# Optimization experiments

Measured on AMD Instinct MI355X. Metric: run time of the kernel, lower is better.

The kernel has to match this reference:

```python
import jax, jax.numpy as jnp
import numpy as np

HIDDEN = 1024
FFN = 3584
NUM_EXPERTS = 8
TOP_K = 2
B, S = 2, 1024


def setup_inputs() -> dict:
    key = jax.random.key(0)
    k0, k1, k2, k3 = jax.random.split(key, 4)
    hidden_states = jax.random.normal(k0, (B, S, HIDDEN), dtype=jnp.float32)
    # torch Linear stores [out, in]; we keep gate as [E, H] (matches nn.Linear weight)
    gate_w = jax.random.normal(k1, (NUM_EXPERTS, HIDDEN), dtype=jnp.float32) * 0.02
    # GroupedLinear weights stored as [E, in, out] for direct x @ W per expert
    w_gate_up = jax.random.normal(k2, (NUM_EXPERTS, HIDDEN, 2 * FFN), dtype=jnp.float32) * 0.02
    w_down = jax.random.normal(k3, (NUM_EXPERTS, FFN, HIDDEN), dtype=jnp.float32) * 0.02
    return {"hidden_states": hidden_states, "gate_w": gate_w,
            "w_gate_up": w_gate_up, "w_down": w_down}


def reference(hidden_states, gate_w, w_gate_up, w_down):
    b, s, h = hidden_states.shape
    x = hidden_states.reshape(-1, h)                      # [T, H]
    T = x.shape[0]
    E = gate_w.shape[0]

    # Router: logits -> fp32 softmax -> top-k -> renormalize (Mixtral semantics)
    router_logits = x @ gate_w.T                          # [T, E]
    probs = jax.nn.softmax(router_logits.astype(jnp.float32), axis=-1)
    top_vals, top_idx = jax.lax.top_k(probs, TOP_K)       # [T, K]
    top_vals = top_vals / top_vals.sum(axis=-1, keepdims=True)
    top_vals = top_vals.astype(x.dtype)

    # Dense combine weights [T, E]: scatter top-k probs to expert slots.
    # Equivalent to permute -> grouped GEMM -> unpermute-with-probs.
    combine = jnp.zeros((T, E), dtype=x.dtype).at[
        jnp.arange(T)[:, None], top_idx].add(top_vals)

    out = jnp.zeros_like(x)
    for e in range(E):  # fixed small expert count
        gu = x @ w_gate_up[e]                             # [T, 2F]
        gate_proj, up_proj = jnp.split(gu, 2, axis=-1)
        act = jax.nn.silu(gate_proj) * up_proj            # [T, F]
        out = out + combine[:, e:e + 1] * (act @ w_down[e])

    return out.reshape(b, s, h), router_logits
```

## Files before the change

### kernel.cpp

```cpp
#include <hip/hip_runtime.h>
#include <hip/hip_bf16.h>
#include <stdint.h>

#define HIDDEN  1024
#define FFN     3584
#define NE      8
#define NTOK    2048
#define CAP     2048
#define OUT_ELEMS (NTOK * HIDDEN)

#define X_OFF    0u
#define CNT_OFF  (4u*1024u*1024u)
#define TOK_OFF  (CNT_OFF + 256u)
#define WGT_OFF  (TOK_OFF + 65536u)
#define INV_OFF  (WGT_OFF + 65536u)
#define ACT_OFF  (INV_OFF + 16384u)
#define ACT_SZ   (4096u * 3584u * 2u)
#define WGU_OFF  (ACT_OFF + ACT_SZ)
#define WGU_SZ   (8u*56u*16u*16384u)
#define WDB_OFF  (WGU_OFF + WGU_SZ)
#define WDB_SZ   (8u*8u*56u*16384u)
#define PART_OFF (WDB_OFF + WDB_SZ)
#define PART_SZ  (4096u*1024u*4u)
#define WS_NEED  ((size_t)PART_OFF + (size_t)PART_SZ)

typedef __attribute__((ext_vector_type(8))) short short8;
typedef __attribute__((ext_vector_type(4))) float floatx4;

static __device__ __forceinline__ uint32_t f2bf(float f) {
  union { float f; uint32_t u; } v; v.f = f;
  return (v.u + 0x7FFFu + ((v.u >> 16) & 1u)) >> 16;
}
static __device__ __forceinline__ uint32_t pack2(float lo, float hi) {
  return f2bf(lo) | (f2bf(hi) << 16);
}
union S8U { uint4 u; short8 s; };
static __device__ __forceinline__ short8 as_short8(uint4 v) { S8U x; x.u = v; return x.s; }

static __device__ __forceinline__ void ld_g2l16(const void* g, void* l) {
  __builtin_amdgcn_global_load_lds(
      (const __attribute__((address_space(1))) void*)g,
      (__attribute__((address_space(3))) void*)l, 16, 0, 0);
}

static __device__ __forceinline__ void stage_tile(
    const char* const* aptr, const char* bptr, size_t akt, size_t bkt,
    uint4* AsB, uint4* BsB, int w)
{
#pragma unroll
  for (int it = 0; it < 4; ++it)
    ld_g2l16(aptr[it] + akt, &AsB[(w * 4 + it) * 64]);
#pragma unroll
  for (int it = 0; it < 4; ++it)
    ld_g2l16(bptr + bkt + (size_t)it * 1024u, &BsB[(w * 4 + it) * 64]);
}

__global__ __launch_bounds__(256) void moe_prep(float4* __restrict__ out4,
                                                int* __restrict__ cnt) {
  uint32_t i = blockIdx.x * 256u + threadIdx.x;
  out4[i] = make_float4(0.f, 0.f, 0.f, 0.f);
  if (blockIdx.x == 0 && threadIdx.x < NE) cnt[threadIdx.x] = 0;
}

__global__ __launch_bounds__(256) void moe_convert(const float4* __restrict__ x4,
                                                   uint4* __restrict__ xb,
                                                   int* __restrict__ cnt) {
  uint32_t g = blockIdx.x * 256u + threadIdx.x;
  float4 a = x4[2u*g], b = x4[2u*g + 1u];
  xb[g] = make_uint4(pack2(a.x, a.y), pack2(a.z, a.w),
                     pack2(b.x, b.y), pack2(b.z, b.w));
  if (blockIdx.x == 0 && threadIdx.x < NE) cnt[threadIdx.x] = 0;
}

__global__ __launch_bounds__(256) void moe_router(
    const float* __restrict__ x, const float* __restrict__ gw,
    float* __restrict__ logits, int* __restrict__ cnt,
    int* __restrict__ tok, float* __restrict__ wgt, int* __restrict__ inv)
{
  const int t = blockIdx.x * 4 + (threadIdx.x >> 6);
  const int lane = threadIdx.x & 63;
  const float* xr = x + (size_t)t * HIDDEN;
  float a[NE];
#pragma unroll
  for (int e = 0; e < NE; ++e) a[e] = 0.f;
  for (int hh = 0; hh < HIDDEN / 64; ++hh) {
    float xv = xr[hh * 64 + lane];
#pragma unroll
    for (int e = 0; e < NE; ++e) a[e] += xv * gw[e * HIDDEN + hh * 64 + lane];
  }
#pragma unroll
  for (int off = 32; off > 0; off >>= 1) {
#pragma unroll
    for (int e = 0; e < NE; ++e) a[e] += __shfl_xor(a[e], off);
  }
  if (lane == 0) {
#pragma unroll
    for (int e = 0; e < NE; ++e) logits[t * NE + e] = a[e];
    int i0 = 0; float v0 = a[0];
#pragma unroll
    for (int e = 1; e < NE; ++e) if (a[e] > v0) { v0 = a[e]; i0 = e; }
    int i1 = (i0 == 0) ? 1 : 0; float v1 = a[i1];
#pragma unroll
    for (int e = 0; e < NE; ++e) if (e != i0 && a[e] > v1) { v1 = a[e]; i1 = e; }
    float w0 = 1.f / (1.f + __expf(v1 - v0));
    float w1 = 1.f - w0;
    int p0 = atomicAdd(&cnt[i0], 1); tok[i0 * CAP + p0] = t; wgt[i0 * CAP + p0] = w0;
    int p1 = atomicAdd(&cnt[i1], 1); tok[i1 * CAP + p1] = t; wgt[i1 * CAP + p1] = w1;
    inv[t * 2 + 0] = i0 * CAP + p0;
    inv[t * 2 + 1] = i1 * CAP + p1;
  }
}

__global__ __launch_bounds__(256) void moe_wconv_gu(const float* __restrict__ wgu,
                                                    uint4* __restrict__ wgub) {
  const int kt = blockIdx.x, fb = blockIdx.y, e = blockIdx.z;
  const int f0 = fb * 64, k0 = kt * 64;
  const float* wB = wgu + (size_t)e * HIDDEN * (2 * FFN);
  uint4* dst = wgub + ((size_t)(e * 56 + fb) * 16 + kt) * 1024;
#pragma unroll
  for (int it = 0; it < 4; ++it) {
    int mid = it * 256 + threadIdx.x;
    int kp = mid >> 5;
    int n  = (mid & 31) * 4;
    int col = f0 + ((n >> 6) << 5) + (n & 31) + (((n >> 5) & 1) ? FFN : 0);
    const float* src = wB + (size_t)(k0 + 2 * kp) * (2 * FFN) + col;
    float4 r0 = *(const float4*)src;
    float4 r1 = *(const float4*)(src + 2 * FFN);
    dst[kp * 32 + ((n >> 2) ^ (((kp >> 2) & 1) << 2))] =
        make_uint4(pack2(r0.x, r1.x), pack2(r0.y, r1.y),
                   pack2(r0.z, r1.z), pack2(r0.w, r1.w));
  }
}

__global__ __launch_bounds__(256) void moe_wconv_d(const float* __restrict__ wd,
                                                   uint4* __restrict__ wdb) {
  const int kt = blockIdx.x, nb = blockIdx.y, e = blockIdx.z;
  const int n0 = nb * 128, k0 = kt * 64;
  const float* wB = wd + (size_t)e * FFN * HIDDEN;
  uint4* dst = wdb + ((size_t)(e * 8 + nb) * 56 + kt) * 1024;
#pragma unroll
  for (int it = 0; it < 4; ++it) {
    int mid = it * 256 + threadIdx.x;
    int kp = mid >> 5;
    int n  = (mid & 31) * 4;
    const float* src = wB + (size_t)(k0 + 2 * kp) * HIDDEN + n0 + n;
    float4 r0 = *(const float4*)src;
    float4 r1 = *(const float4*)(src + HIDDEN);
    dst[kp * 32 + ((n >> 2) ^ (((kp >> 2) & 1) << 2))] =
        make_uint4(pack2(r0.x, r1.x), pack2(r0.y, r1.y),
                   pack2(r0.z, r1.z), pack2(r0.w, r1.w));
  }
}

__global__ __launch_bounds__(256) void moe_gateup(
    const uint4* __restrict__ xb, const uint4* __restrict__ wgub,
    const int* __restrict__ cnt, const int* __restrict__ tok,
    unsigned short* __restrict__ act)
{
  const int e  = blockIdx.z;
  const int m0 = blockIdx.y * 128;
  const int fb = blockIdx.x;
  const int f0 = fb * 64;
  const int cn = cnt[e];
  if (m0 >= cn) return;
  int basev = 0;
#pragma unroll
  for (int i = 0; i < NE; ++i) { int ci = cnt[i]; if (i < e) basev += ci; }

  __shared__ uint4 As[2][1024];
  __shared__ uint4 Bs4[2][1024];

  const int tid  = threadIdx.x;
  const int lane = tid & 63;
  const int w    = tid >> 6;
  const int wm   = w >> 1, wn = w & 1;
  const int q    = lane >> 4;
  const int c    = lane & 15;

  const int* tokE = tok + e * CAP;
  const char* aptr[4];
#pragma unroll
  for (int it = 0; it < 4; ++it) {
    int p   = (w * 4 + it) * 64 + lane;
    int row = p >> 3, c8 = p & 7;
    int mrow = m0 + row; if (mrow >= cn) mrow = cn - 1;
    aptr[it] = (const char*)(xb + (size_t)tokE[mrow] * (HIDDEN / 8) + (c8 ^ (row & 7)));
  }
  const char* bptr = (const char*)wgub + ((size_t)(e * 56 + fb) * 16) * 16384u
                   + (size_t)w * 4096u + (size_t)lane * 16u;

  floatx4 acc[4][4];
#pragma unroll
  for (int i = 0; i < 4; ++i)
#pragma unroll
    for (int j = 0; j < 4; ++j) acc[i][j] = (floatx4){0.f, 0.f, 0.f, 0.f};

  const int NT = HIDDEN / 64;
  stage_tile(aptr, bptr, 0, 0, As[0], Bs4[0], w);
  __syncthreads();
  int cur = 0;
  for (int kt = 0; kt < NT; ++kt) {
    if (kt + 1 < NT)
      stage_tile(aptr, bptr, (size_t)(kt + 1) * 128u, (size_t)(kt + 1) * 16384u,
                 As[cur ^ 1], Bs4[cur ^ 1], w);
    const uint4*    Asc = As[cur];
    const uint32_t* Bsc = (const uint32_t*)Bs4[cur];
#pragma unroll
    for (int ks = 0; ks < 2; ++ks) {
      short8 af[4];
#pragma unroll
      for (int i = 0; i < 4; ++i) {
        int row = wm * 64 + i * 16 + c;
        int kc8 = ks * 4 + q;
        af[i] = as_short8(Asc[row * 8 + (kc8 ^ (row & 7))]);
      }
      short8 bfr[4];
#pragma unroll
      for (int j = 0; j < 4; ++j) {
        int n  = wn * 64 + j * 16 + c;
        int kp = ks * 16 + q * 4;
        int nn = n ^ ((q & 1) << 4);
        bfr[j] = as_short8(make_uint4(Bsc[(kp + 0) * 128 + nn], Bsc[(kp + 1) * 128 + nn],
                                      Bsc[(kp + 2) * 128 + nn], Bsc[(kp + 3) * 128 + nn]));
      }
#pragma unroll
      for (int i = 0; i < 4; ++i)
#pragma unroll
        for (int j = 0; j < 4; ++j)
          acc[i][j] = __builtin_amdgcn_mfma_f32_16x16x32_bf16(af[i], bfr[j], acc[i][j], 0, 0, 0);
    }
    __syncthreads();
    cur ^= 1;
  }

#pragma unroll
  for (int i = 0; i < 4; ++i) {
#pragma unroll
    for (int r = 0; r < 4; ++r) {
      int m = m0 + wm * 64 + i * 16 + q * 4 + r;
      if (m < cn) {
#pragma unroll
        for (int j = 0; j < 2; ++j) {
          float g = acc[i][j][r];
          float u = acc[i][j + 2][r];
          float a = (g / (1.f + __expf(-g))) * u;
          act[(size_t)(basev + m) * FFN + (f0 + wn * 32 + j * 16 + c)] = (unsigned short)f2bf(a);
        }
      }
    }
  }
}

__global__ __launch_bounds__(256) void moe_down(
    const unsigned short* __restrict__ act, const uint4* __restrict__ wdb,
    const int* __restrict__ cnt, const int* __restrict__ tok,
    const float* __restrict__ wgt, float* __restrict__ part)
{
  const int e  = blockIdx.z;
  const int m0 = blockIdx.y * 128;
  const int nb = blockIdx.x;
  const int n0 = nb * 128;
  const int cn = cnt[e];
  if (m0 >= cn) return;
  int basev = 0;
#pragma unroll
  for (int i = 0; i < NE; ++i) { int ci = cnt[i]; if (i < e) basev += ci; }

  __shared__ uint4 As[2][1024];
  __shared__ uint4 Bs4[2][1024];

  const int tid  = threadIdx.x;
  const int lane = tid & 63;
  const int w    = tid >> 6;
  const int wm   = w >> 1, wn = w & 1;
  const int q    = lane >> 4;
  const int c    = lane & 15;

  const char* aptr[4];
#pragma unroll
  for (int it = 0; it < 4; ++it) {
    int p   = (w * 4 + it) * 64 + lane;
    int row = p >> 3, c8 = p & 7;
    int mrow = m0 + row; if (mrow >= cn) mrow = cn - 1;
    aptr[it] = (const char*)act +
               ((size_t)(basev + mrow) * FFN + (size_t)((c8 ^ (row & 7)) * 8)) * 2u;
  }
  const char* bptr = (const char*)wdb + ((size_t)(e * 8 + nb) * 56) * 16384u
                   + (size_t)w * 4096u + (size_t)lane * 16u;

  floatx4 acc[4][4];
#pragma unroll
  for (int i = 0; i < 4; ++i)
#pragma unroll
    for (int j = 0; j < 4; ++j) acc[i][j] = (floatx4){0.f, 0.f, 0.f, 0.f};

  const int NT = FFN / 64;
  stage_tile(aptr, bptr, 0, 0, As[0], Bs4[0], w);
  __syncthreads();
  int cur = 0;
  for (int kt = 0; kt < NT; ++kt) {
    if (kt + 1 < NT)
      stage_tile(aptr, bptr, (size_t)(kt + 1) * 128u, (size_t)(kt + 1) * 16384u,
                 As[cur ^ 1], Bs4[cur ^ 1], w);
    const uint4*    Asc = As[cur];
    const uint32_t* Bsc = (const uint32_t*)Bs4[cur];
#pragma unroll
    for (int ks = 0; ks < 2; ++ks) {
      short8 af[4];
#pragma unroll
      for (int i = 0; i < 4; ++i) {
        int row = wm * 64 + i * 16 + c;
        int kc8 = ks * 4 + q;
        af[i] = as_short8(Asc[row * 8 + (kc8 ^ (row & 7))]);
      }
      short8 bfr[4];
#pragma unroll
      for (int j = 0; j < 4; ++j) {
        int n  = wn * 64 + j * 16 + c;
        int kp = ks * 16 + q * 4;
        int nn = n ^ ((q & 1) << 4);
        bfr[j] = as_short8(make_uint4(Bsc[(kp + 0) * 128 + nn], Bsc[(kp + 1) * 128 + nn],
                                      Bsc[(kp + 2) * 128 + nn], Bsc[(kp + 3) * 128 + nn]));
      }
#pragma unroll
      for (int i = 0; i < 4; ++i)
#pragma unroll
        for (int j = 0; j < 4; ++j)
          acc[i][j] = __builtin_amdgcn_mfma_f32_16x16x32_bf16(af[i], bfr[j], acc[i][j], 0, 0, 0);
    }
    __syncthreads();
    cur ^= 1;
  }

#pragma unroll
  for (int i = 0; i < 4; ++i) {
#pragma unroll
    for (int r = 0; r < 4; ++r) {
      int m = m0 + wm * 64 + i * 16 + q * 4 + r;
      if (m < cn) {
        float  wg   = wgt[e * CAP + m];
        float* prow = part + (size_t)(basev + m) * HIDDEN + n0 + wn * 64 + c;
#pragma unroll
        for (int j = 0; j < 4; ++j)
          prow[j * 16] = acc[i][j][r] * wg;
      }
    }
  }
}

__global__ __launch_bounds__(256) void moe_combine(
    const int* __restrict__ cnt, const int* __restrict__ inv,
    const float4* __restrict__ part4, float4* __restrict__ out4)
{
  const int t  = blockIdx.x;
  const int s0 = inv[2 * t], s1 = inv[2 * t + 1];
  const int e0 = s0 >> 11, e1 = s1 >> 11;
  int b0 = 0, b1 = 0;
#pragma unroll
  for (int i = 0; i < NE; ++i) {
    int ci = cnt[i];
    if (i < e0) b0 += ci;
    if (i < e1) b1 += ci;
  }
  const size_t r0 = (size_t)(b0 + (s0 & (CAP - 1))) * 256u;
  const size_t r1 = (size_t)(b1 + (s1 & (CAP - 1))) * 256u;
  const int i = threadIdx.x;
  float4 a = part4[r0 + i];
  float4 b = part4[r1 + i];
  out4[(size_t)t * 256u + i] = make_float4(a.x + b.x, a.y + b.y, a.z + b.z, a.w + b.w);
}

__global__ __launch_bounds__(256) void moe_gateup_lg(
    const uint4* __restrict__ xb, const float* __restrict__ wgu,
    const int* __restrict__ cnt, const int* __restrict__ tok,
    unsigned short* __restrict__ act)
{
  const int e  = blockIdx.z;
  const int m0 = blockIdx.y * 128;
  const int f0 = blockIdx.x * 64;
  const int cn = cnt[e];
  if (m0 >= cn) return;
  int basev = 0;
#pragma unroll
  for (int i = 0; i < NE; ++i) { int ci = cnt[i]; if (i < e) basev += ci; }

  __shared__ uint4    As[1024];
  __shared__ uint32_t Bs[4096];

  const int tid  = threadIdx.x;
  const int lane = tid & 63;
  const int w    = tid >> 6;
  const int wm   = w >> 1, wn = w & 1;
  const int q    = lane >> 4;
  const int c    = lane & 15;

  floatx4 acc[4][4];
#pragma unroll
  for (int i = 0; i < 4; ++i)
#pragma unroll
    for (int j = 0; j < 4; ++j) acc[i][j] = (floatx4){0.f, 0.f, 0.f, 0.f};

  const float* wB  = wgu + (size_t)e * HIDDEN * (2 * FFN);
  const int* tokE  = tok + e * CAP;

  for (int kt = 0; kt < HIDDEN / 64; ++kt) {
    const int k0 = kt * 64;
    __syncthreads();
#pragma unroll
    for (int it = 0; it < 4; ++it) {
      int cid = it * 256 + tid;
      int row = cid >> 3, c8 = cid & 7;
      int mrow = m0 + row; if (mrow >= cn) mrow = cn - 1;
      int tk = tokE[mrow];
      As[row * 8 + (c8 ^ (row & 7))] = xb[(size_t)tk * (HIDDEN / 8) + (k0 >> 3) + c8];
    }
#pragma unroll
    for (int it = 0; it < 4; ++it) {
      int mid = it * 256 + tid;
      int kp = mid >> 5;
      int n  = (mid & 31) * 4;
      int col = f0 + ((n >> 6) << 5) + (n & 31) + (((n >> 5) & 1) ? FFN : 0);
      const float* src = wB + (size_t)(k0 + 2 * kp) * (2 * FFN) + col;
      float4 r0 = *(const float4*)src;
      float4 r1 = *(const float4*)(src + 2 * FFN);
      int widx = kp * 128 + (n ^ (((kp >> 2) & 1) << 4));
      *(uint4*)&Bs[widx] = make_uint4(pack2(r0.x, r1.x), pack2(r0.y, r1.y),
                                      pack2(r0.z, r1.z), pack2(r0.w, r1.w));
    }
    __syncthreads();
#pragma unroll
    for (int ks = 0; ks < 2; ++ks) {
      short8 af[4];
#pragma unroll
      for (int i = 0; i < 4; ++i) {
        int row = wm * 64 + i * 16 + c;
        int kc8 = ks * 4 + q;
        af[i] = as_short8(As[row * 8 + (kc8 ^ (row & 7))]);
      }
      short8 bfr[4];
#pragma unroll
      for (int j = 0; j < 4; ++j) {
        int n  = wn * 64 + j * 16 + c;
        int kp = ks * 16 + q * 4;
        int nn = n ^ ((q & 1) << 4);
        bfr[j] = as_short8(make_uint4(Bs[(kp + 0) * 128 + nn], Bs[(kp + 1) * 128 + nn],
                                      Bs[(kp + 2) * 128 + nn], Bs[(kp + 3) * 128 + nn]));
      }
#pragma unroll
      for (int i = 0; i < 4; ++i)
#pragma unroll
        for (int j = 0; j < 4; ++j)
          acc[i][j] = __builtin_amdgcn_mfma_f32_16x16x32_bf16(af[i], bfr[j], acc[i][j], 0, 0, 0);
    }
  }

#pragma unroll
  for (int i = 0; i < 4; ++i) {
#pragma unroll
    for (int r = 0; r < 4; ++r) {
      int m = m0 + wm * 64 + i * 16 + q * 4 + r;
      if (m < cn) {
#pragma unroll
        for (int j = 0; j < 2; ++j) {
          float g = acc[i][j][r];
          float u = acc[i][j + 2][r];
          float a = (g / (1.f + __expf(-g))) * u;
          act[(size_t)(basev + m) * FFN + (f0 + wn * 32 + j * 16 + c)] = (unsigned short)f2bf(a);
        }
      }
    }
  }
}

__global__ __launch_bounds__(256) void moe_down_lg(
    const uint4* __restrict__ actc, const float* __restrict__ wd,
    const int* __restrict__ cnt, const int* __restrict__ tok,
    const float* __restrict__ wgt, float* __restrict__ out)
{
  const int e  = blockIdx.z;
  const int m0 = blockIdx.y * 128;
  const int n0 = blockIdx.x * 128;
  const int cn = cnt[e];
  if (m0 >= cn) return;
  int basev = 0;
#pragma unroll
  for (int i = 0; i < NE; ++i) { int ci = cnt[i]; if (i < e) basev += ci; }

  __shared__ uint4    As[1024];
  __shared__ uint32_t Bs[4096];

  const int tid  = threadIdx.x;
  const int lane = tid & 63;
  const int w    = tid >> 6;
  const int wm   = w >> 1, wn = w & 1;
  const int q    = lane >> 4;
  const int c    = lane & 15;

  floatx4 acc[4][4];
#pragma unroll
  for (int i = 0; i < 4; ++i)
#pragma unroll
    for (int j = 0; j < 4; ++j) acc[i][j] = (floatx4){0.f, 0.f, 0.f, 0.f};

  const float* wB = wd + (size_t)e * FFN * HIDDEN;

  for (int kt = 0; kt < FFN / 64; ++kt) {
    const int k0 = kt * 64;
    __syncthreads();
#pragma unroll
    for (int it = 0; it < 4; ++it) {
      int cid = it * 256 + tid;
      int row = cid >> 3, c8 = cid & 7;
      int mrow = m0 + row; if (mrow >= cn) mrow = cn - 1;
      As[row * 8 + (c8 ^ (row & 7))] =
          actc[(size_t)(basev + mrow) * (FFN / 8) + (k0 >> 3) + c8];
    }
#pragma unroll
    for (int it = 0; it < 4; ++it) {
      int mid = it * 256 + tid;
      int kp = mid >> 5;
      int n  = (mid & 31) * 4;
      int col = n0 + n;
      const float* src = wB + (size_t)(k0 + 2 * kp) * HIDDEN + col;
      float4 r0 = *(const float4*)src;
      float4 r1 = *(const float4*)(src + HIDDEN);
      int widx = kp * 128 + (n ^ (((kp >> 2) & 1) << 4));
      *(uint4*)&Bs[widx] = make_uint4(pack2(r0.x, r1.x), pack2(r0.y, r1.y),
                                      pack2(r0.z, r1.z), pack2(r0.w, r1.w));
    }
    __syncthreads();
#pragma unroll
    for (int ks = 0; ks < 2; ++ks) {
      short8 af[4];
#pragma unroll
      for (int i = 0; i < 4; ++i) {
        int row = wm * 64 + i * 16 + c;
        int kc8 = ks * 4 + q;
        af[i] = as_short8(As[row * 8 + (kc8 ^ (row & 7))]);
      }
      short8 bfr[4];
#pragma unroll
      for (int j = 0; j < 4; ++j) {
        int n  = wn * 64 + j * 16 + c;
        int kp = ks * 16 + q * 4;
        int nn = n ^ ((q & 1) << 4);
        bfr[j] = as_short8(make_uint4(Bs[(kp + 0) * 128 + nn], Bs[(kp + 1) * 128 + nn],
                                      Bs[(kp + 2) * 128 + nn], Bs[(kp + 3) * 128 + nn]));
      }
#pragma unroll
      for (int i = 0; i < 4; ++i)
#pragma unroll
        for (int j = 0; j < 4; ++j)
          acc[i][j] = __builtin_amdgcn_mfma_f32_16x16x32_bf16(af[i], bfr[j], acc[i][j], 0, 0, 0);
    }
  }

#pragma unroll
  for (int i = 0; i < 4; ++i) {
#pragma unroll
    for (int r = 0; r < 4; ++r) {
      int m = m0 + wm * 64 + i * 16 + q * 4 + r;
      if (m < cn) {
        int   t  = tok[e * CAP + m];
        float wg = wgt[e * CAP + m];
        float* orow = out + (size_t)t * HIDDEN + n0 + wn * 64 + c;
#pragma unroll
        for (int j = 0; j < 4; ++j)
          atomicAdd(orow + j * 16, acc[i][j][r] * wg);
      }
    }
  }
}

extern "C" void kernel_launch(void* const* d_in, const int* in_sizes, int n_in,
                              void* d_out, int out_size, void* d_ws, size_t ws_size,
                              hipStream_t stream)
{
  (void)in_sizes; (void)n_in; (void)out_size;
  const float* x   = (const float*)d_in[0];
  const float* gw  = (const float*)d_in[1];
  const float* wgu = (const float*)d_in[2];
  const float* wd  = (const float*)d_in[3];
  float* out = (float*)d_out;
  char*  ws  = (char*)d_ws;

  uint4*          xb   = (uint4*)(ws + X_OFF);
  int*            cnt  = (int*)(ws + CNT_OFF);
  int*            tok  = (int*)(ws + TOK_OFF);
  float*          wgt  = (float*)(ws + WGT_OFF);
  int*            inv  = (int*)(ws + INV_OFF);
  unsigned short* act  = (unsigned short*)(ws + ACT_OFF);
  uint4*          wgub = (uint4*)(ws + WGU_OFF);
  uint4*          wdb  = (uint4*)(ws + WDB_OFF);
  float*          part = (float*)(ws + PART_OFF);

  const bool fast = (ws_size >= WS_NEED);

  if (fast) {
    moe_convert<<<(NTOK * HIDDEN) / (256 * 8), 256, 0, stream>>>((const float4*)x, xb, cnt);
    moe_router<<<NTOK / 4, 256, 0, stream>>>(x, gw, out + OUT_ELEMS, cnt, tok, wgt, inv);
    moe_wconv_gu<<<dim3(16, 56, NE), 256, 0, stream>>>(wgu, wgub);
    moe_wconv_d<<<dim3(56, 8, NE), 256, 0, stream>>>(wd, wdb);
    moe_gateup<<<dim3(FFN / 64, 16, NE), 256, 0, stream>>>(xb, wgub, cnt, tok, act);
    moe_down<<<dim3(HIDDEN / 128, 16, NE), 256, 0, stream>>>(act, wdb, cnt, tok, wgt, part);
    moe_combine<<<NTOK, 256, 0, stream>>>(cnt, inv, (const float4*)part, (float4*)out);
  } else {
    moe_prep<<<OUT_ELEMS / (256 * 4), 256, 0, stream>>>((float4*)out, cnt);
    moe_convert<<<(NTOK * HIDDEN) / (256 * 8), 256, 0, stream>>>((const float4*)x, xb, cnt);
    moe_router<<<NTOK / 4, 256, 0, stream>>>(x, gw, out + OUT_ELEMS, cnt, tok, wgt, inv);
    moe_gateup_lg<<<dim3(FFN / 64, 16, NE), 256, 0, stream>>>(xb, wgu, cnt, tok, act);
    moe_down_lg<<<dim3(HIDDEN / 128, 16, NE), 256, 0, stream>>>((const uint4*)act, wd, cnt, tok, wgt, out);
  }
}
```

Measured before the change: 676.8 us.

## Store converted bf16 weights N-major so B fragments load as one 16-byte LDS read

The weight conversion kernels now transpose each 64x128 fp32 tile through padded shared memory and write bf16 weights in an N-major, K-contiguous swizzled layout matching the A operand. The GEMM inner loops then read each B fragment with a single 128-bit LDS load instead of four 32-bit loads. This cuts LDS instruction count in both the gate-up and down GEMMs. In exchange, the conversion kernels gain an LDS round trip and a barrier.

```diff
diff --git a/kernel.cpp b/kernel.cpp
--- a/kernel.cpp
+++ b/kernel.cpp
@@ -117,18 +117,30 @@
   const int f0 = fb * 64, k0 = kt * 64;
   const float* wB = wgu + (size_t)e * HIDDEN * (2 * FFN);
   uint4* dst = wgub + ((size_t)(e * 56 + fb) * 16 + kt) * 1024;
-#pragma unroll
-  for (int it = 0; it < 4; ++it) {
-    int mid = it * 256 + threadIdx.x;
-    int kp = mid >> 5;
-    int n  = (mid & 31) * 4;
-    int col = f0 + ((n >> 6) << 5) + (n & 31) + (((n >> 5) & 1) ? FFN : 0);
-    const float* src = wB + (size_t)(k0 + 2 * kp) * (2 * FFN) + col;
-    float4 r0 = *(const float4*)src;
-    float4 r1 = *(const float4*)(src + 2 * FFN);
-    dst[kp * 32 + ((n >> 2) ^ (((kp >> 2) & 1) << 2))] =
-        make_uint4(pack2(r0.x, r1.x), pack2(r0.y, r1.y),
-                   pack2(r0.z, r1.z), pack2(r0.w, r1.w));
+
+  __shared__ float lds_f[64 * 129];
+
+#pragma unroll
+  for (int p = 0; p < 8; ++p) {
+    int idx = p * 256 + threadIdx.x;
+    int r   = idx >> 5;
+    int lc  = (idx & 31) * 4;
+    int col = f0 + ((lc >> 6) << 5) + (lc & 31) + (((lc >> 5) & 1) ? FFN : 0);
+    float4 v = *(const float4*)(wB + (size_t)(k0 + r) * (2 * FFN) + col);
+    float* d = &lds_f[r * 129 + lc];
+    d[0] = v.x; d[1] = v.y; d[2] = v.z; d[3] = v.w;
+  }
+  __syncthreads();
+#pragma unroll
+  for (int p = 0; p < 4; ++p) {
+    int m  = p * 256 + threadIdx.x;
+    int ne = m >> 3, c8 = m & 7;
+    float f[8];
+#pragma unroll
+    for (int kk = 0; kk < 8; ++kk) f[kk] = lds_f[(c8 * 8 + kk) * 129 + ne];
+    dst[ne * 8 + (c8 ^ (ne & 7))] =
+        make_uint4(pack2(f[0], f[1]), pack2(f[2], f[3]),
+                   pack2(f[4], f[5]), pack2(f[6], f[7]));
   }
 }
 
@@ -138,17 +150,29 @@
   const int n0 = nb * 128, k0 = kt * 64;
   const float* wB = wd + (size_t)e * FFN * HIDDEN;
   uint4* dst = wdb + ((size_t)(e * 8 + nb) * 56 + kt) * 1024;
-#pragma unroll
-  for (int it = 0; it < 4; ++it) {
-    int mid = it * 256 + threadIdx.x;
-    int kp = mid >> 5;
-    int n  = (mid & 31) * 4;
-    const float* src = wB + (size_t)(k0 + 2 * kp) * HIDDEN + n0 + n;
-    float4 r0 = *(const float4*)src;
-    float4 r1 = *(const float4*)(src + HIDDEN);
-    dst[kp * 32 + ((n >> 2) ^ (((kp >> 2) & 1) << 2))] =
-        make_uint4(pack2(r0.x, r1.x), pack2(r0.y, r1.y),
-                   pack2(r0.z, r1.z), pack2(r0.w, r1.w));
+
+  __shared__ float lds_f[64 * 129];
+
+#pragma unroll
+  for (int p = 0; p < 8; ++p) {
+    int idx = p * 256 + threadIdx.x;
+    int r   = idx >> 5;
+    int lc  = (idx & 31) * 4;
+    float4 v = *(const float4*)(wB + (size_t)(k0 + r) * HIDDEN + n0 + lc);
+    float* d = &lds_f[r * 129 + lc];
+    d[0] = v.x; d[1] = v.y; d[2] = v.z; d[3] = v.w;
+  }
+  __syncthreads();
+#pragma unroll
+  for (int p = 0; p < 4; ++p) {
+    int m  = p * 256 + threadIdx.x;
+    int ne = m >> 3, c8 = m & 7;
+    float f[8];
+#pragma unroll
+    for (int kk = 0; kk < 8; ++kk) f[kk] = lds_f[(c8 * 8 + kk) * 129 + ne];
+    dst[ne * 8 + (c8 ^ (ne & 7))] =
+        make_uint4(pack2(f[0], f[1]), pack2(f[2], f[3]),
+                   pack2(f[4], f[5]), pack2(f[6], f[7]));
   }
 }
 
@@ -203,25 +227,22 @@
     if (kt + 1 < NT)
       stage_tile(aptr, bptr, (size_t)(kt + 1) * 128u, (size_t)(kt + 1) * 16384u,
                  As[cur ^ 1], Bs4[cur ^ 1], w);
-    const uint4*    Asc = As[cur];
-    const uint32_t* Bsc = (const uint32_t*)Bs4[cur];
+    const uint4* Asc = As[cur];
+    const uint4* Bsc = Bs4[cur];
 #pragma unroll
     for (int ks = 0; ks < 2; ++ks) {
+      const int kc8 = ks * 4 + q;
       short8 af[4];
 #pragma unroll
       for (int i = 0; i < 4; ++i) {
         int row = wm * 64 + i * 16 + c;
-        int kc8 = ks * 4 + q;
         af[i] = as_short8(Asc[row * 8 + (kc8 ^ (row & 7))]);
       }
       short8 bfr[4];
 #pragma unroll
       for (int j = 0; j < 4; ++j) {
-        int n  = wn * 64 + j * 16 + c;
-        int kp = ks * 16 + q * 4;
-        int nn = n ^ ((q & 1) << 4);
-        bfr[j] = as_short8(make_uint4(Bsc[(kp + 0) * 128 + nn], Bsc[(kp + 1) * 128 + nn],
-                                      Bsc[(kp + 2) * 128 + nn], Bsc[(kp + 3) * 128 + nn]));
+        int n = wn * 64 + j * 16 + c;
+        bfr[j] = as_short8(Bsc[n * 8 + (kc8 ^ (n & 7))]);
       }
 #pragma unroll
       for (int i = 0; i < 4; ++i)
@@ -302,25 +323,22 @@
     if (kt + 1 < NT)
       stage_tile(aptr, bptr, (size_t)(kt + 1) * 128u, (size_t)(kt + 1) * 16384u,
                  As[cur ^ 1], Bs4[cur ^ 1], w);
-    const uint4*    Asc = As[cur];
-    const uint32_t* Bsc = (const uint32_t*)Bs4[cur];
+    const uint4* Asc = As[cur];
+    const uint4* Bsc = Bs4[cur];
 #pragma unroll
     for (int ks = 0; ks < 2; ++ks) {
+      const int kc8 = ks * 4 + q;
       short8 af[4];
 #pragma unroll
       for (int i = 0; i < 4; ++i) {
         int row = wm * 64 + i * 16 + c;
-        int kc8 = ks * 4 + q;
         af[i] = as_short8(Asc[row * 8 + (kc8 ^ (row & 7))]);
       }
       short8 bfr[4];
 #pragma unroll
       for (int j = 0; j < 4; ++j) {
-        int n  = wn * 64 + j * 16 + c;
-        int kp = ks * 16 + q * 4;
-        int nn = n ^ ((q & 1) << 4);
-        bfr[j] = as_short8(make_uint4(Bsc[(kp + 0) * 128 + nn], Bsc[(kp + 1) * 128 + nn],
-                                      Bsc[(kp + 2) * 128 + nn], Bsc[(kp + 3) * 128 + nn]));
+        int n = wn * 64 + j * 16 + c;
+        bfr[j] = as_short8(Bsc[n * 8 + (kc8 ^ (n & 7))]);
       }
 #pragma unroll
       for (int i = 0; i < 4; ++i)
```

New measurement: 664.5 us. No clear change (-1.8%).
